# Optimization experiments

Measured on AMD Instinct MI355X. Metric: run time of the kernel, lower is better.

Reference implementation:

```python
import jax, jax.numpy as jnp
import numpy as np

B, T, D_MODEL, D_HEAD = 8, 2048, 1024, 64


def setup_inputs() -> dict:
    key = jax.random.key(0)
    kx, kq, kk, kv = jax.random.split(key, 4)
    s = 1.0 / np.sqrt(D_MODEL)
    return {
        "x": jax.random.normal(kx, (B, T, D_MODEL), dtype=jnp.float32),
        "W_Q": jax.random.normal(kq, (D_MODEL, D_HEAD), dtype=jnp.float32) * s,
        "W_K": jax.random.normal(kk, (D_MODEL, D_HEAD), dtype=jnp.float32) * s,
        "W_V": jax.random.normal(kv, (D_MODEL, D_HEAD), dtype=jnp.float32) * s,
    }


def reference(x, W_Q, W_K, W_V):
    # x: [B, T, d_model]; projections -> [B, T, d_head]
    q = jnp.einsum("btd,dh->bth", x, W_Q)
    k = jnp.einsum("btd,dh->bth", x, W_K)
    v = jnp.einsum("btd,dh->bth", x, W_V)
    d_head = W_Q.shape[-1]
    scale = 1.0 / jnp.sqrt(jnp.asarray(d_head, dtype=x.dtype))
    # scores: [B, T, T], causal mask (lower-triangular kept)
    scores = jnp.einsum("bqh,bkh->bqk", q, k) * scale
    T_ = x.shape[1]
    causal = jnp.tril(jnp.ones((T_, T_), dtype=bool))
    scores = jnp.where(causal[None, :, :], scores, jnp.asarray(-jnp.inf, dtype=x.dtype))
    a = jax.nn.softmax(scores, axis=-1)
    # dropout omitted (eval mode / identity)
    out = jnp.einsum("bqk,bkh->bqh", a, v)
    return out
```

## Files before the change

### kernel.cpp

```cpp
#include <hip/hip_runtime.h>

#define TT   2048
#define DM   1024
#define DH   64
#define NB   8
#define KST  72

typedef __attribute__((ext_vector_type(4))) float          f32x4;
typedef __attribute__((ext_vector_type(4))) int            i32x4;
typedef __attribute__((ext_vector_type(4))) unsigned short u16x4;
typedef __attribute__((ext_vector_type(8))) short          s16x8;

__device__ __forceinline__ unsigned short f2bf(float f) {
  unsigned int u = __float_as_uint(f);
  u += 0x7fffu + ((u >> 16) & 1u);
  return (unsigned short)(u >> 16);
}

#define MFMA(acc, a, b) \
  (acc) = __builtin_amdgcn_mfma_f32_16x16x32_bf16((a), (b), (acc), 0, 0, 0)

__device__ __forceinline__ void gload_lds16(const void* g, void* l) {
  __builtin_amdgcn_global_load_lds(
      (const __attribute__((address_space(1))) void*)g,
      (__attribute__((address_space(3))) void*)l, 16, 0, 0);
}

#define WS_WT    0u
#define WS_QK    393216u
#define WS_VT    4587520u
#define WS_OP    6684672u
#define WS_ML    16121856u

__global__ __launch_bounds__(256) void pack_w_kernel(
    const float* __restrict__ wq, const float* __restrict__ wk,
    const float* __restrict__ wv, unsigned short* __restrict__ wt) {
  int idx = blockIdx.x * 256 + threadIdx.x;
  if (idx >= 192 * DM) return;
  int n = idx >> 10;
  int k = idx & (DM - 1);
  const float* src = (n < 64) ? wq : ((n < 128) ? wk : wv);
  wt[(size_t)n * DM + k] = f2bf(src[(size_t)k * DH + (n & 63)]);
}

__global__ __launch_bounds__(256) void qkv_gemm_kernel(
    const float* __restrict__ x, const unsigned short* __restrict__ wt,
    unsigned short* __restrict__ qkvqk, unsigned short* __restrict__ vt) {
  __shared__ __align__(16) float          a_lds[32 * 64];
  __shared__ __align__(16) unsigned short b_lds[192 * 64];

  const int tid  = threadIdx.x;
  const int lane = tid & 63;
  const int w    = tid >> 6;
  const int ln   = lane & 15;
  const int quad = lane >> 4;
  const int mw   = w & 1;
  const int nw   = w >> 1;
  const int m0   = blockIdx.x * 32;
  const int n0   = nw * 96;
  const int lsw  = ln & 7;

  int agoff[2];
  #pragma unroll
  for (int i = 0; i < 2; ++i) {
    int s = i * 256 + w * 64 + lane;
    int m = s >> 4, cc = s & 15;
    agoff[i] = (m0 + m) * DM + ((cc ^ (m & 7)) << 2);
  }
  int bgoff[6];
  #pragma unroll
  for (int j = 0; j < 6; ++j) {
    int s = j * 256 + w * 64 + lane;
    int n = s >> 3, cc = s & 7;
    bgoff[j] = n * DM + ((cc ^ (n & 7)) << 3);
  }

  f32x4 acc[6];
  #pragma unroll
  for (int i = 0; i < 6; ++i) acc[i] = (f32x4){0.f, 0.f, 0.f, 0.f};
  union { s16x8 v; unsigned short h[8]; } ap;

  #pragma unroll
  for (int i = 0; i < 2; ++i)
    gload_lds16(x + agoff[i], (void*)(a_lds + (i * 256 + w * 64) * 4));
  #pragma unroll
  for (int j = 0; j < 6; ++j)
    gload_lds16(wt + bgoff[j], (void*)(b_lds + (j * 256 + w * 64) * 8));

  for (int k0 = 0; k0 < DM; k0 += 64) {
    __syncthreads();
    #pragma unroll
    for (int ks = 0; ks < 64; ks += 32) {
      const int m  = mw * 16 + ln;
      const int c0 = (ks >> 2) + 2 * quad;
      f32x4 v0 = *(const f32x4*)&a_lds[m * 64 + ((c0 ^ lsw) << 2)];
      f32x4 v1 = *(const f32x4*)&a_lds[m * 64 + (((c0 + 1) ^ lsw) << 2)];
      #pragma unroll
      for (int j = 0; j < 4; ++j) { ap.h[j] = f2bf(v0[j]); ap.h[4 + j] = f2bf(v1[j]); }
      s16x8 af = ap.v;
      const int cb = (ks >> 3) + quad;
      #pragma unroll
      for (int nt = 0; nt < 6; ++nt) {
        int n = n0 + nt * 16 + ln;
        s16x8 bf = *(const s16x8*)&b_lds[n * 64 + ((cb ^ lsw) << 3)];
        MFMA(acc[nt], af, bf);
      }
    }
    __syncthreads();
    if (k0 + 64 < DM) {
      const int kn = k0 + 64;
      #pragma unroll
      for (int i = 0; i < 2; ++i)
        gload_lds16(x + agoff[i] + kn, (void*)(a_lds + (i * 256 + w * 64) * 4));
      #pragma unroll
      for (int j = 0; j < 6; ++j)
        gload_lds16(wt + bgoff[j] + kn, (void*)(b_lds + (j * 256 + w * 64) * 8));
    }
  }

  const float QS = 0.18033688011112042f;
  const int mm0 = m0 + mw * 16;
  const int bz  = mm0 >> 11;
  const int tb  = (mm0 & 2047) + quad * 4;
  #pragma unroll
  for (int nt = 0; nt < 6; ++nt) {
    const int ncol = n0 + nt * 16 + ln;
    if (ncol < 128) {
      const float sc = (ncol < 64) ? QS : 1.0f;
      #pragma unroll
      for (int r = 0; r < 4; ++r) {
        int row = mm0 + quad * 4 + r;
        qkvqk[(size_t)row * 128 + ncol] = f2bf(acc[nt][r] * sc);
      }
    } else {
      int d = ncol - 128;
      u16x4 h;
      #pragma unroll
      for (int r = 0; r < 4; ++r) h[r] = f2bf(acc[nt][r]);
      *(u16x4*)(vt + ((size_t)bz * 64 + d) * TT + tb) = h;
    }
  }
}

__global__ __launch_bounds__(256) void attn_part_kernel(
    const unsigned short* __restrict__ qkvqk, const unsigned short* __restrict__ vt,
    unsigned short* __restrict__ opart, float* __restrict__ ml) {
  const int Ctab[16] = {0,1,2,4,6,9,12,16,20,25,30,36,42,49,56,64};
  const int f  = blockIdx.x;
  const int bz = f / 72;
  const int rw = f - bz * 72;
  int s = 0;
  #pragma unroll
  for (int t = 1; t < 16; ++t) if (rw >= Ctab[t]) s = t;
  const int c = rw - Ctab[s];
  const int ntiles = min(4, 2 * s + 2 - 4 * c);
  const int qtA = 2 * s, qtB = 2 * s + 1;

  __shared__ __align__(16) unsigned short k_lds[256 * 64];
  __shared__ __align__(16) unsigned short v_lds[64 * 256];
  __shared__ __align__(16) unsigned short p_lds[64 * KST];

  const int tid  = threadIdx.x;
  const int w    = tid >> 6;
  const int lane = tid & 63;
  const int ln   = lane & 15;
  const int quad = lane >> 4;
  const int lsw  = ln & 7;
  const int bb   = bz * TT;
  const int kbase = c * 256;

  #pragma unroll
  for (int i = 0; i < 8; ++i) {
    int base = (i * 4 + w) * 64;
    int slot = base + lane;
    int row = slot >> 3, cc = slot & 7;
    gload_lds16(qkvqk + (size_t)(bb + kbase + row) * 128 + 64 + ((cc ^ (row & 7)) << 3),
                (void*)(k_lds + base * 8));
  }
  #pragma unroll
  for (int i = 0; i < 8; ++i) {
    int base = (i * 4 + w) * 64;
    int slot = base + lane;
    int d = slot >> 5, cc = slot & 31;
    gload_lds16(vt + ((size_t)bz * 64 + d) * TT + kbase + ((cc ^ (d & 7)) << 3),
                (void*)(v_lds + base * 8));
  }

  const unsigned short* qrowA = qkvqk + (size_t)(bb + qtA * 64 + w * 16 + ln) * 128;
  const unsigned short* qrowB = qrowA + 64 * 128;
  const s16x8 qfA0 = *(const s16x8*)(qrowA + quad * 8);
  const s16x8 qfA1 = *(const s16x8*)(qrowA + 32 + quad * 8);
  const s16x8 qfB0 = *(const s16x8*)(qrowB + quad * 8);
  const s16x8 qfB1 = *(const s16x8*)(qrowB + 32 + quad * 8);

  s16x8 ones;
  #pragma unroll
  for (int j = 0; j < 8; ++j) ones[j] = (short)0x3F80;

  f32x4 acc_oA[4], acc_oB[4], acc_lA, acc_lB;
  #pragma unroll
  for (int i = 0; i < 4; ++i) {
    acc_oA[i] = (f32x4){0.f, 0.f, 0.f, 0.f};
    acc_oB[i] = (f32x4){0.f, 0.f, 0.f, 0.f};
  }
  acc_lA = (f32x4){0.f, 0.f, 0.f, 0.f};
  acc_lB = (f32x4){0.f, 0.f, 0.f, 0.f};

  const int qgA = qtA * 64 + w * 16 + quad * 4;
  const int qgB = qgA + 64;
  __syncthreads();

  for (int ct = 0; ct < ntiles; ++ct) {
    const int ktg = c * 4 + ct;
    const int kc0 = quad;
    const int kc1 = 4 + quad;

    if (ktg <= qtA) {
      const bool diag = (ktg == qtA);
      f32x4 acc_s[4];
      #pragma unroll
      for (int i = 0; i < 4; ++i) acc_s[i] = (f32x4){0.f, 0.f, 0.f, 0.f};
      #pragma unroll
      for (int ns = 0; ns < 4; ++ns) {
        const int krow = ct * 64 + ns * 16 + ln;
        s16x8 kf0 = *(const s16x8*)&k_lds[krow * 64 + ((kc0 ^ lsw) << 3)];
        s16x8 kf1 = *(const s16x8*)&k_lds[krow * 64 + ((kc1 ^ lsw) << 3)];
        MFMA(acc_s[ns], qfA0, kf0);
        MFMA(acc_s[ns], qfA1, kf1);
      }
      #pragma unroll
      for (int r = 0; r < 4; ++r) {
        const int qg = qgA + r;
        #pragma unroll
        for (int ns = 0; ns < 4; ++ns) {
          float sv = acc_s[ns][r];
          if (diag) {
            int kg = ktg * 64 + ns * 16 + ln;
            sv = (kg <= qg) ? sv : -1e30f;
          }
          p_lds[(w * 16 + quad * 4 + r) * KST + ns * 16 + ln] = f2bf(exp2f(sv));
        }
      }
      #pragma unroll
      for (int kk = 0; kk < 64; kk += 32) {
        s16x8 pf = *(const s16x8*)&p_lds[(w * 16 + ln) * KST + kk + quad * 8];
        MFMA(acc_lA, pf, ones);
        #pragma unroll
        for (int nt = 0; nt < 4; ++nt) {
          const int d  = nt * 16 + ln;
          const int sc = ct * 8 + (((kk >> 3) + quad) ^ lsw);
          s16x8 vf = *(const s16x8*)&v_lds[d * 256 + sc * 8];
          MFMA(acc_oA[nt], pf, vf);
        }
      }
      asm volatile("" ::: "memory");
    }

    {
      const bool diag = (ktg == qtB);
      f32x4 acc_s[4];
      #pragma unroll
      for (int i = 0; i < 4; ++i) acc_s[i] = (f32x4){0.f, 0.f, 0.f, 0.f};
      #pragma unroll
      for (int ns = 0; ns < 4; ++ns) {
        const int krow = ct * 64 + ns * 16 + ln;
        s16x8 kf0 = *(const s16x8*)&k_lds[krow * 64 + ((kc0 ^ lsw) << 3)];
        s16x8 kf1 = *(const s16x8*)&k_lds[krow * 64 + ((kc1 ^ lsw) << 3)];
        MFMA(acc_s[ns], qfB0, kf0);
        MFMA(acc_s[ns], qfB1, kf1);
      }
      #pragma unroll
      for (int r = 0; r < 4; ++r) {
        const int qg = qgB + r;
        #pragma unroll
        for (int ns = 0; ns < 4; ++ns) {
          float sv = acc_s[ns][r];
          if (diag) {
            int kg = ktg * 64 + ns * 16 + ln;
            sv = (kg <= qg) ? sv : -1e30f;
          }
          p_lds[(w * 16 + quad * 4 + r) * KST + ns * 16 + ln] = f2bf(exp2f(sv));
        }
      }
      #pragma unroll
      for (int kk = 0; kk < 64; kk += 32) {
        s16x8 pf = *(const s16x8*)&p_lds[(w * 16 + ln) * KST + kk + quad * 8];
        MFMA(acc_lB, pf, ones);
        #pragma unroll
        for (int nt = 0; nt < 4; ++nt) {
          const int d  = nt * 16 + ln;
          const int sc = ct * 8 + (((kk >> 3) + quad) ^ lsw);
          s16x8 vf = *(const s16x8*)&v_lds[d * 256 + sc * 8];
          MFMA(acc_oB[nt], pf, vf);
        }
      }
      asm volatile("" ::: "memory");
    }
  }

  #pragma unroll
  for (int half = 0; half < 2; ++half) {
    const int qt = (half == 0) ? qtA : qtB;
    const int g  = qt >> 2, rq = qt & 3;
    const int base = qt + 2 * g * (g - 1) + rq * g;
    const size_t slab = (size_t)bz * 144 + base + c;
    unsigned short* op = opart + slab * 4096;
    const f32x4* ao = (half == 0) ? acc_oA : acc_oB;
    const f32x4  al = (half == 0) ? acc_lA : acc_lB;
    #pragma unroll
    for (int nt = 0; nt < 4; ++nt)
      #pragma unroll
      for (int r = 0; r < 4; ++r)
        op[(w * 16 + quad * 4 + r) * 64 + nt * 16 + ln] = f2bf(ao[nt][r]);
    if (ln == 0) {
      float* lp = ml + slab * 64;
      #pragma unroll
      for (int r = 0; r < 4; ++r)
        lp[w * 16 + quad * 4 + r] = al[r];
    }
  }
}

__global__ __launch_bounds__(256) void attn_combine_kernel(
    const unsigned short* __restrict__ opart, const float* __restrict__ ml,
    float* __restrict__ out) {
  const int qt = blockIdx.x;
  const int bz = blockIdx.y;
  const int aq = qt >> 2, rq = qt & 3;
  const int nch = aq + 1;
  const int base = qt + 2 * aq * (aq - 1) + rq * aq;
  const size_t slab0 = (size_t)bz * 144 + base;

  const int tid = threadIdx.x;
  const int row = tid >> 2;
  const int ds  = (tid & 3) * 16;

  float L = 0.f;
  float acc[16];
  #pragma unroll
  for (int j = 0; j < 16; ++j) acc[j] = 0.f;
  #pragma unroll 8
  for (int ch = 0; ch < nch; ++ch) {
    L += ml[(slab0 + ch) * 64 + row];
    const unsigned short* op = opart + (slab0 + ch) * 4096 + row * 64 + ds;
    i32x4 v0 = *(const i32x4*)(op);
    i32x4 v1 = *(const i32x4*)(op + 8);
    #pragma unroll
    for (int j = 0; j < 4; ++j) {
      unsigned int u0 = (unsigned int)v0[j], u1 = (unsigned int)v1[j];
      acc[j * 2]         += __uint_as_float(u0 << 16);
      acc[j * 2 + 1]     += __uint_as_float(u0 & 0xffff0000u);
      acc[8 + j * 2]     += __uint_as_float(u1 << 16);
      acc[8 + j * 2 + 1] += __uint_as_float(u1 & 0xffff0000u);
    }
  }
  float inv = 1.0f / L;
  float* o = out + ((size_t)bz * TT + qt * 64 + row) * 64 + ds;
  #pragma unroll
  for (int j = 0; j < 16; ++j) o[j] = acc[j] * inv;
}

extern "C" void kernel_launch(void* const* d_in, const int* in_sizes, int n_in,
                              void* d_out, int out_size, void* d_ws, size_t ws_size,
                              hipStream_t stream) {
  const float* x  = (const float*)d_in[0];
  const float* wq = (const float*)d_in[1];
  const float* wk = (const float*)d_in[2];
  const float* wv = (const float*)d_in[3];
  float* out = (float*)d_out;

  char* ws = (char*)d_ws;
  unsigned short* wt    = (unsigned short*)(ws + WS_WT);
  unsigned short* qkvqk = (unsigned short*)(ws + WS_QK);
  unsigned short* vt    = (unsigned short*)(ws + WS_VT);
  unsigned short* opart = (unsigned short*)(ws + WS_OP);
  float*          ml    = (float*)(ws + WS_ML);

  pack_w_kernel<<<(192 * DM + 255) / 256, 256, 0, stream>>>(wq, wk, wv, wt);
  qkv_gemm_kernel<<<NB * TT / 32, 256, 0, stream>>>(x, wt, qkvqk, vt);
  attn_part_kernel<<<NB * 72, 256, 0, stream>>>(qkvqk, vt, opart, ml);
  attn_combine_kernel<<<dim3(32, NB), 256, 0, stream>>>(opart, ml, out);
}
```

Before: 144.2 us.

## Split-K the QKV projection GEMM into two halves with a separate reduce kernel

The QKV projection GEMM is split along the reduction dimension into two halves, launched as a 512x2 grid that writes fp32 partial sums to a workspace buffer. A new reduce kernel adds the two partials, applies the Q scale, converts to bf16 and writes both the QK layout and the transposed V layout. The aim is to double the number of blocks in flight so that more CUs stay busy during the projection. In exchange it adds about 25 MB of fp32 partial-sum traffic and one more kernel launch.

```diff
diff --git a/kernel.cpp b/kernel.cpp
--- a/kernel.cpp
+++ b/kernel.cpp
@@ -4,6 +4,7 @@
 #define DM   1024
 #define DH   64
 #define NB   8
+#define KS   512
 #define KST  72
 
 typedef __attribute__((ext_vector_type(4))) float          f32x4;
@@ -31,6 +32,7 @@
 #define WS_VT    4587520u
 #define WS_OP    6684672u
 #define WS_ML    16121856u
+#define WS_P     16416768u
 
 __global__ __launch_bounds__(256) void pack_w_kernel(
     const float* __restrict__ wq, const float* __restrict__ wk,
@@ -45,7 +47,7 @@
 
 __global__ __launch_bounds__(256) void qkv_gemm_kernel(
     const float* __restrict__ x, const unsigned short* __restrict__ wt,
-    unsigned short* __restrict__ qkvqk, unsigned short* __restrict__ vt) {
+    float* __restrict__ pbuf) {
   __shared__ __align__(16) float          a_lds[32 * 64];
   __shared__ __align__(16) unsigned short b_lds[192 * 64];
 
@@ -58,6 +60,7 @@
   const int nw   = w >> 1;
   const int m0   = blockIdx.x * 32;
   const int n0   = nw * 96;
+  const int ks0  = blockIdx.y * KS;
   const int lsw  = ln & 7;
 
   int agoff[2];
@@ -65,14 +68,14 @@
   for (int i = 0; i < 2; ++i) {
     int s = i * 256 + w * 64 + lane;
     int m = s >> 4, cc = s & 15;
-    agoff[i] = (m0 + m) * DM + ((cc ^ (m & 7)) << 2);
+    agoff[i] = (m0 + m) * DM + ks0 + ((cc ^ (m & 7)) << 2);
   }
   int bgoff[6];
   #pragma unroll
   for (int j = 0; j < 6; ++j) {
     int s = j * 256 + w * 64 + lane;
     int n = s >> 3, cc = s & 7;
-    bgoff[j] = n * DM + ((cc ^ (n & 7)) << 3);
+    bgoff[j] = n * DM + ks0 + ((cc ^ (n & 7)) << 3);
   }
 
   f32x4 acc[6];
@@ -87,7 +90,7 @@
   for (int j = 0; j < 6; ++j)
     gload_lds16(wt + bgoff[j], (void*)(b_lds + (j * 256 + w * 64) * 8));
 
-  for (int k0 = 0; k0 < DM; k0 += 64) {
+  for (int k0 = 0; k0 < KS; k0 += 64) {
     __syncthreads();
     #pragma unroll
     for (int ks = 0; ks < 64; ks += 32) {
@@ -107,7 +110,7 @@
       }
     }
     __syncthreads();
-    if (k0 + 64 < DM) {
+    if (k0 + 64 < KS) {
       const int kn = k0 + 64;
       #pragma unroll
       for (int i = 0; i < 2; ++i)
@@ -118,27 +121,54 @@
     }
   }
 
-  const float QS = 0.18033688011112042f;
+  float* pp = pbuf + (size_t)blockIdx.y * 16384 * 192;
   const int mm0 = m0 + mw * 16;
-  const int bz  = mm0 >> 11;
-  const int tb  = (mm0 & 2047) + quad * 4;
   #pragma unroll
   for (int nt = 0; nt < 6; ++nt) {
     const int ncol = n0 + nt * 16 + ln;
-    if (ncol < 128) {
-      const float sc = (ncol < 64) ? QS : 1.0f;
-      #pragma unroll
-      for (int r = 0; r < 4; ++r) {
-        int row = mm0 + quad * 4 + r;
-        qkvqk[(size_t)row * 128 + ncol] = f2bf(acc[nt][r] * sc);
-      }
-    } else {
-      int d = ncol - 128;
-      u16x4 h;
-      #pragma unroll
-      for (int r = 0; r < 4; ++r) h[r] = f2bf(acc[nt][r]);
-      *(u16x4*)(vt + ((size_t)bz * 64 + d) * TT + tb) = h;
-    }
+    #pragma unroll
+    for (int r = 0; r < 4; ++r) {
+      int row = mm0 + quad * 4 + r;
+      pp[(size_t)row * 192 + ncol] = acc[nt][r];
+    }
+  }
+}
+
+__global__ __launch_bounds__(256) void qkv_reduce_kernel(
+    const float* __restrict__ pbuf, unsigned short* __restrict__ qkvqk,
+    unsigned short* __restrict__ vt) {
+  const float* p0 = pbuf;
+  const float* p1 = pbuf + (size_t)16384 * 192;
+  const float QS = 0.18033688011112042f;
+  int id = blockIdx.x * 256 + threadIdx.x;
+
+  if (blockIdx.x < 1024) {
+    int row = id >> 4;
+    int c8  = (id & 15) * 8;
+    size_t o = (size_t)row * 192 + c8;
+    f32x4 s0 = *(const f32x4*)(p0 + o)     + *(const f32x4*)(p1 + o);
+    f32x4 s1 = *(const f32x4*)(p0 + o + 4) + *(const f32x4*)(p1 + o + 4);
+    const float sc = (c8 < 64) ? QS : 1.0f;
+    u16x4 h0, h1;
+    #pragma unroll
+    for (int j = 0; j < 4; ++j) { h0[j] = f2bf(s0[j] * sc); h1[j] = f2bf(s1[j] * sc); }
+    *(u16x4*)(qkvqk + (size_t)row * 128 + c8)     = h0;
+    *(u16x4*)(qkvqk + (size_t)row * 128 + c8 + 4) = h1;
+  } else {
+    int v  = id - 262144;
+    int b  = v >> 14;
+    int d  = (v >> 8) & 63;
+    int t8 = (v & 255) * 8;
+    u16x4 h0, h1;
+    #pragma unroll
+    for (int j = 0; j < 8; ++j) {
+      size_t o = (size_t)(b * TT + t8 + j) * 192 + 128 + d;
+      float s = p0[o] + p1[o];
+      if (j < 4) h0[j] = f2bf(s); else h1[j - 4] = f2bf(s);
+    }
+    unsigned short* dst = vt + ((size_t)b * 64 + d) * TT + t8;
+    *(u16x4*)(dst)     = h0;
+    *(u16x4*)(dst + 4) = h1;
   }
 }
 
@@ -375,9 +405,11 @@
   unsigned short* vt    = (unsigned short*)(ws + WS_VT);
   unsigned short* opart = (unsigned short*)(ws + WS_OP);
   float*          ml    = (float*)(ws + WS_ML);
+  float*          pbuf  = (float*)(ws + WS_P);
 
   pack_w_kernel<<<(192 * DM + 255) / 256, 256, 0, stream>>>(wq, wk, wv, wt);
-  qkv_gemm_kernel<<<NB * TT / 32, 256, 0, stream>>>(x, wt, qkvqk, vt);
+  qkv_gemm_kernel<<<dim3(512, 2), 256, 0, stream>>>(x, wt, pbuf);
+  qkv_reduce_kernel<<<1536, 256, 0, stream>>>(pbuf, qkvqk, vt);
   attn_part_kernel<<<NB * 72, 256, 0, stream>>>(qkvqk, vt, opart, ml);
   attn_combine_kernel<<<dim3(32, NB), 256, 0, stream>>>(opart, ml, out);
 }
```

Result: slower. 162.7 us (+12.9%).
